# Kernel tuning notes

Hardware: AMD Instinct MI355X
Metric: run time of the kernel (lower is better)

Reference implementation:

```python
import jax, jax.numpy as jnp
import numpy as np

B, L, D, H, HID = 2048, 512, 17, 8, 256  # batch, max entities, feat dim, heads, mlp hidden
SPECIAL, OUT = 9, 23  # special vector dims, policy logits (7+16)


def _lin(k, out_d, in_d, scale):
    kw, kb = jax.random.split(k)
    W = jax.random.normal(kw, (out_d, in_d), jnp.float32) * scale
    b = jax.random.normal(kb, (out_d,), jnp.float32) * 0.01
    return W, b


def setup_inputs() -> dict:
    key = jax.random.key(0)
    ks = jax.random.split(key, 16)
    # observations: row 0 holds the 9-dim special vector, rows 1..L are ragged entities
    x = jax.random.normal(ks[0], (B, L + 1, D), jnp.float32)
    lengths = jax.random.randint(ks[1], (B,), 1, L + 1)
    mask = (jnp.arange(L)[None, :] < lengths[:, None]).astype(jnp.float32)
    x = x.at[:, 1:, :].multiply(mask[:, :, None])  # zero rows mark padding
    s = 1.0 / np.sqrt(D)
    # per-head K/V projections (num_heads separate tiny Linears)
    Wk = jax.random.normal(ks[2], (H, D, D), jnp.float32) * s
    bk = jax.random.normal(ks[3], (H, D), jnp.float32) * 0.01
    Wv = jax.random.normal(ks[4], (H, D, D), jnp.float32) * s
    bv = jax.random.normal(ks[5], (H, D), jnp.float32) * 0.01
    q = jax.random.normal(ks[6], (H, D), jnp.float32)  # learned per-head queries
    Wo, bo = _lin(ks[7], D, H * D, 1.0 / np.sqrt(H * D))
    sc = 1.0 / np.sqrt(D + SPECIAL)
    pW1, pb1 = _lin(ks[8], HID, D + SPECIAL, sc)
    pW2, pb2 = _lin(ks[9], HID, HID, 1.0 / np.sqrt(HID))
    pW3, pb3 = _lin(ks[10], OUT, HID, 1.0 / np.sqrt(HID))
    vW1, vb1 = _lin(ks[11], HID, D + SPECIAL, sc)
    vW2, vb2 = _lin(ks[12], HID, HID, 1.0 / np.sqrt(HID))
    vW3, vb3 = _lin(ks[13], 1, HID, 1.0 / np.sqrt(HID))
    return dict(x=x, Wk=Wk, bk=bk, Wv=Wv, bv=bv, q=q, Wo=Wo, bo=bo,
                pW1=pW1, pb1=pb1, pW2=pW2, pb2=pb2, pW3=pW3, pb3=pb3,
                vW1=vW1, vb1=vb1, vW2=vW2, vb2=vb2, vW3=vW3, vb3=vb3)


def _mlp(h, W1, b1, W2, b2, W3, b3):
    h = jax.nn.relu(h @ W1.T + b1)
    h = jax.nn.relu(h @ W2.T + b2)
    return h @ W3.T + b3


def reference(x, Wk, bk, Wv, bv, q, Wo, bo,
              pW1, pb1, pW2, pb2, pW3, pb3,
              vW1, vb1, vW2, vb2, vW3, vb3):
    special = x[:, 0, :SPECIAL]            # [B, 9]
    seq = x[:, 1:, :]                      # [B, L, D]
    mask = jnp.sum(jnp.abs(seq), axis=-1) != 0  # [B, L] non-padded rows
    # per-head keys/values for all samples at once (batched over the head loop)
    keys = jnp.einsum('bld,hed->bhle', seq, Wk) + bk[None, :, None, :]   # [B,H,L,D]
    vals = jnp.einsum('bld,hed->bhle', seq, Wv) + bv[None, :, None, :]   # [B,H,L,D]
    scores = jnp.einsum('bhle,he->bhl', keys, q)                          # [B,H,L]
    scores = jnp.where(mask[:, None, :], scores, -1e9)
    w = jax.nn.softmax(scores, axis=-1)                                   # [B,H,L]
    agg = jnp.einsum('bhl,bhle->bhe', w, vals).reshape(x.shape[0], H * D)  # concat heads
    attn = agg @ Wo.T + bo                                                # [B, D]
    comb = jnp.concatenate([attn, special], axis=-1)                      # [B, D+9]
    logits = _mlp(comb, pW1, pb1, pW2, pb2, pW3, pb3)                     # [B, 23]
    value = _mlp(comb, vW1, vb1, vW2, vb2, vW3, vb3)                      # [B, 1]
    return logits, value
```

## Files before the change

### kernel.cpp

```cpp
#include <hip/hip_runtime.h>
#include <hip/hip_bf16.h>

#define B_ 2048
#define D_ 17
#define H_ 8
#define HID_ 256
#define OUT_ 23
#define XROW 8721
#define SEQN 8704

__device__ __forceinline__ float4 ld4u(const float* p) {
  float4 v; __builtin_memcpy(&v, p, 16); return v;
}

__global__ __launch_bounds__(256) void prep_kernel(
    const float* __restrict__ pW2, const float* __restrict__ vW2,
    const float* __restrict__ Wk, const float* __restrict__ bk,
    const float* __restrict__ q,
    float* __restrict__ pW2t, float* __restrict__ vW2t, float* __restrict__ qkc)
{
  const int bid = blockIdx.x;
  const int t = threadIdx.x;
  if (bid == 128) {
    if (t < H_ * D_) {
      const int h = t / D_, dd = t - h * D_;
      float s = 0.f;
      #pragma unroll
      for (int e = 0; e < D_; ++e) s = fmaf(Wk[h*289 + e*D_ + dd], q[h*D_ + e], s);
      qkc[h*18 + dd] = s;
    } else if (t < H_ * D_ + H_) {
      const int h = t - H_ * D_;
      float s = 0.f;
      #pragma unroll
      for (int e = 0; e < D_; ++e) s = fmaf(bk[h*D_ + e], q[h*D_ + e], s);
      qkc[h*18 + 17] = s;
    }
    return;
  }
  __shared__ float tile[32][33];
  const int m = bid >> 6, tid = bid & 63;
  const int ti = (tid >> 3) * 32, tk = (tid & 7) * 32;
  const float* src = m ? vW2 : pW2;
  float* dst = m ? vW2t : pW2t;
  const int tx = t & 31, ty = t >> 5;
  #pragma unroll
  for (int r = 0; r < 4; ++r) tile[ty + 8*r][tx] = src[(ti + ty + 8*r)*HID_ + tk + tx];
  __syncthreads();
  #pragma unroll
  for (int r = 0; r < 4; ++r) dst[(tk + ty + 8*r)*HID_ + ti + tx] = tile[tx][ty + 8*r];
}

__global__ __launch_bounds__(256, 4) void attn_comb_kernel(
    const float* __restrict__ x, const float* __restrict__ qkc,
    const float* __restrict__ Wv, const float* __restrict__ bv,
    const float* __restrict__ Wo, const float* __restrict__ bo,
    float* __restrict__ comb)
{
  __shared__ float smem[9688];
  float* s_seq  = smem;
  float* s_part = smem + 8704;
  float* s_swn  = smem + 9280;
  float* s_agg  = smem + 9416;
  float* s_wp   = smem + 9552;

  const int t = threadIdx.x;
  const int b = blockIdx.x;
  const int w = t >> 6, lane = t & 63;
  const int h = lane & 7, rg = lane >> 3;
  const float* xb = x + (size_t)b * XROW;
  const float* xs = xb + D_;

  const float pv = xs[lane * 136];
  unsigned long long live = __ballot(pv != 0.f) | 1ull;
  const int ptop = 63 - __builtin_clzll(live);
  const int nrows = 8 * (ptop + 1);
  const int ng = nrows >> 2;

  {
    const int rounds = (nrows * D_ + 1023) >> 10;
    float4 tmp[9];
    #pragma unroll
    for (int j = 0; j < 9; ++j) {
      if (j < rounds) {
        int off = (j * 256 + t) * 4;
        if (off > SEQN - 4) off = SEQN - 4;
        tmp[j] = ld4u(xs + off);
      }
    }
    #pragma unroll
    for (int j = 0; j < 9; ++j) {
      if (j < rounds) *(float4*)&s_seq[(j * 256 + t) * 4] = tmp[j];
    }
  }

  float qk[D_];
  #pragma unroll
  for (int d = 0; d < D_; ++d) qk[d] = qkc[h*18 + d];
  const float chr = qkc[h*18 + 17];

  __syncthreads();

  float den = 0.f, acc[D_];
  #pragma unroll
  for (int d = 0; d < D_; ++d) acc[d] = 0.f;

  auto dorow = [&](const float* r, bool ok) {
    float sc = chr;
    #pragma unroll
    for (int d = 0; d < D_; ++d) sc = fmaf(qk[d], r[d], sc);
    const float p = (ok && r[0] != 0.f) ? __expf(sc) : 0.f;
    den += p;
    #pragma unroll
    for (int d = 0; d < D_; ++d) acc[d] = fmaf(p, r[d], acc[d]);
  };

  #pragma unroll 1
  for (int g0 = w * 8; g0 < ng; g0 += 32) {
    const int g = g0 + rg;
    const bool okg = (g < ng);
    const float* gb = &s_seq[(okg ? g : (ng - 1)) * 68];
    {
      float fA[36];
      #pragma unroll
      for (int i = 0; i < 9; ++i) {
        const float4 v = *(const float4*)(gb + 4*i);
        fA[4*i] = v.x; fA[4*i+1] = v.y; fA[4*i+2] = v.z; fA[4*i+3] = v.w;
      }
      dorow(&fA[0], okg);
      dorow(&fA[17], okg);
    }
    {
      float fB[36];
      #pragma unroll
      for (int i = 0; i < 9; ++i) {
        const float4 v = *(const float4*)(gb + 32 + 4*i);
        fB[4*i] = v.x; fB[4*i+1] = v.y; fB[4*i+2] = v.z; fB[4*i+3] = v.w;
      }
      dorow(&fB[2], okg);
      dorow(&fB[19], okg);
    }
  }

  #pragma unroll
  for (int m = 8; m <= 32; m <<= 1) {
    den += __shfl_xor(den, m, 64);
    #pragma unroll
    for (int d = 0; d < D_; ++d) acc[d] += __shfl_xor(acc[d], m, 64);
  }
  if (lane < 8) {
    float* pp = &s_part[(w * 8 + lane) * 18];
    pp[0] = den;
    #pragma unroll
    for (int d = 0; d < D_; ++d) pp[1 + d] = acc[d];
  }
  __syncthreads();

  if (t < 136) {
    const int hh = t / D_, d = t - hh * D_;
    float dn = 0.f, ac = 0.f;
    #pragma unroll
    for (int ww = 0; ww < 4; ++ww) {
      const float* pp = &s_part[(ww * 8 + hh) * 18];
      dn += pp[0]; ac += pp[1 + d];
    }
    s_swn[hh * D_ + d] = ac / dn;
  }
  __syncthreads();
  if (t < 136) {
    const int hh = t / D_, e = t - hh * D_;
    float s = bv[hh*D_ + e];
    #pragma unroll
    for (int d = 0; d < D_; ++d) s = fmaf(Wv[hh*289 + e*D_ + d], s_swn[hh*D_ + d], s);
    s_agg[hh*D_ + e] = s;
  }
  __syncthreads();
  if (t < 136) {
    const int o = t >> 3, pt = t & 7;
    float s = 0.f;
    #pragma unroll
    for (int j = 0; j < D_; ++j) s = fmaf(Wo[o*136 + pt*D_ + j], s_agg[pt*D_ + j], s);
    s_wp[t] = s;
  }
  __syncthreads();
  if (t < D_) {
    float s = bo[t];
    #pragma unroll
    for (int pt = 0; pt < 8; ++pt) s += s_wp[t*8 + pt];
    comb[b*26 + t] = s;
  } else if (t < 26) {
    comb[b*26 + t] = xb[t - D_];
  }
}

__global__ __launch_bounds__(512) void mlp_kernel(
    const float* __restrict__ comb,
    const float* __restrict__ pW1, const float* __restrict__ pb1,
    const float* __restrict__ pW2t, const float* __restrict__ pb2,
    const float* __restrict__ pW3, const float* __restrict__ pb3,
    const float* __restrict__ vW1, const float* __restrict__ vb1,
    const float* __restrict__ vW2t, const float* __restrict__ vb2,
    const float* __restrict__ vW3, const float* __restrict__ vb3,
    float* __restrict__ out)
{
  __shared__ float s_comb[8][26];
  __shared__ __align__(16) float s_h1[2][8][HID_];
  __shared__ __align__(16) float s_h2[2][8][HID_];

  const int t = threadIdx.x;
  const int b0 = blockIdx.x * 8;
  const int p = t >> 8;
  const int i = t & 255;

  if (t < 208) { const int bb = t / 26, k = t - bb*26; s_comb[bb][k] = comb[(size_t)(b0 + bb)*26 + k]; }
  __syncthreads();

  const float* W1  = p ? vW1  : pW1;   const float* B1 = p ? vb1 : pb1;
  const float* W2t = p ? vW2t : pW2t;  const float* B2 = p ? vb2 : pb2;

  {
    float a[8];
    #pragma unroll
    for (int bb = 0; bb < 8; ++bb) a[bb] = 0.f;
    const float* wr = W1 + i*26;
    for (int k = 0; k < 26; ++k) {
      const float wk = wr[k];
      #pragma unroll
      for (int bb = 0; bb < 8; ++bb) a[bb] = fmaf(wk, s_comb[bb][k], a[bb]);
    }
    const float bias = B1[i];
    #pragma unroll
    for (int bb = 0; bb < 8; ++bb) s_h1[p][bb][i] = fmaxf(a[bb] + bias, 0.f);
  }
  __syncthreads();

  {
    float a[8];
    #pragma unroll
    for (int bb = 0; bb < 8; ++bb) a[bb] = 0.f;
    #pragma unroll 2
    for (int k4 = 0; k4 < 64; ++k4) {
      const int k = 4*k4;
      const float w0 = W2t[(k    )*HID_ + i];
      const float w1 = W2t[(k + 1)*HID_ + i];
      const float w2 = W2t[(k + 2)*HID_ + i];
      const float w3 = W2t[(k + 3)*HID_ + i];
      #pragma unroll
      for (int bb = 0; bb < 8; ++bb) {
        const float4 hv = *(const float4*)&s_h1[p][bb][k];
        a[bb] = fmaf(w0, hv.x, fmaf(w1, hv.y, fmaf(w2, hv.z, fmaf(w3, hv.w, a[bb]))));
      }
    }
    const float bias = B2[i];
    #pragma unroll
    for (int bb = 0; bb < 8; ++bb) s_h2[p][bb][i] = fmaxf(a[bb] + bias, 0.f);
  }
  __syncthreads();

  if (t < 184) {
    const int bb = t / OUT_, o = t - bb * OUT_;
    const float4* w4 = (const float4*)(pW3 + o * HID_);
    const float4* h4 = (const float4*)&s_h2[0][bb][0];
    float s = pb3[o];
    for (int k = 0; k < 64; ++k) {
      const float4 wv = w4[k], hv = h4[k];
      s = fmaf(wv.x, hv.x, fmaf(wv.y, hv.y, fmaf(wv.z, hv.z, fmaf(wv.w, hv.w, s))));
    }
    out[(size_t)(b0 + bb) * OUT_ + o] = s;
  } else if (t >= 256 && t < 264) {
    const int bb = t - 256;
    const float4* w4 = (const float4*)vW3;
    const float4* h4 = (const float4*)&s_h2[1][bb][0];
    float s = vb3[0];
    for (int k = 0; k < 64; ++k) {
      const float4 wv = w4[k], hv = h4[k];
      s = fmaf(wv.x, hv.x, fmaf(wv.y, hv.y, fmaf(wv.z, hv.z, fmaf(wv.w, hv.w, s))));
    }
    out[(size_t)B_ * OUT_ + b0 + bb] = s;
  }
}

extern "C" void kernel_launch(void* const* d_in, const int* in_sizes, int n_in,
                              void* d_out, int out_size, void* d_ws, size_t ws_size,
                              hipStream_t stream) {
  (void)in_sizes; (void)n_in; (void)out_size; (void)ws_size;
  const float* x   = (const float*)d_in[0];
  const float* Wk  = (const float*)d_in[1];
  const float* bk  = (const float*)d_in[2];
  const float* Wv  = (const float*)d_in[3];
  const float* bv  = (const float*)d_in[4];
  const float* q   = (const float*)d_in[5];
  const float* Wo  = (const float*)d_in[6];
  const float* bo  = (const float*)d_in[7];
  const float* pW1 = (const float*)d_in[8];
  const float* pb1 = (const float*)d_in[9];
  const float* pW2 = (const float*)d_in[10];
  const float* pb2 = (const float*)d_in[11];
  const float* pW3 = (const float*)d_in[12];
  const float* pb3 = (const float*)d_in[13];
  const float* vW1 = (const float*)d_in[14];
  const float* vb1 = (const float*)d_in[15];
  const float* vW2 = (const float*)d_in[16];
  const float* vb2 = (const float*)d_in[17];
  const float* vW3 = (const float*)d_in[18];
  const float* vb3 = (const float*)d_in[19];
  float* out = (float*)d_out;

  float* comb = (float*)d_ws;
  float* pW2t = comb + (size_t)B_ * 26;
  float* vW2t = pW2t + (size_t)HID_ * HID_;
  float* qkc  = vW2t + (size_t)HID_ * HID_;

  prep_kernel<<<129, 256, 0, stream>>>(pW2, vW2, Wk, bk, q, pW2t, vW2t, qkc);
  attn_comb_kernel<<<B_, 256, 0, stream>>>(x, qkc, Wv, bv, Wo, bo, comb);
  mlp_kernel<<<B_ / 8, 512, 0, stream>>>(comb, pW1, pb1, pW2t, pb2, pW3, pb3,
                                         vW1, vb1, vW2t, vb2, vW3, vb3, out);
}
```

Baseline: 57.48 us.

## Batch four samples per attention block with double-buffered loads; restructure MLP layer 2

The attention kernel now handles four samples per 512-thread block. It prefetches the next sample's sequence into registers while computing the current one and writes it into a second shared buffer, so global loads overlap with compute. The MLP second layer is rewritten as split-K. Each wave broadcasts its 64 hidden values through readlane, loads float4 weight columns, and the partial sums are reduced through shared memory. The trade-off is more shared memory and registers per block and fewer blocks in the attention grid, which may lower occupancy.

```diff
diff --git a/kernel.cpp b/kernel.cpp
--- a/kernel.cpp
+++ b/kernel.cpp
@@ -8,9 +8,13 @@
 #define OUT_ 23
 #define XROW 8721
 #define SEQN 8704
+#define NB 4
 
 __device__ __forceinline__ float4 ld4u(const float* p) {
   float4 v; __builtin_memcpy(&v, p, 16); return v;
+}
+__device__ __forceinline__ float bclane(float v, int l) {
+  return __uint_as_float(__builtin_amdgcn_readlane(__float_as_uint(v), l));
 }
 
 __global__ __launch_bounds__(256) void prep_kernel(
@@ -50,47 +54,29 @@
   for (int r = 0; r < 4; ++r) dst[(tk + ty + 8*r)*HID_ + ti + tx] = tile[tx][ty + 8*r];
 }
 
-__global__ __launch_bounds__(256, 4) void attn_comb_kernel(
+__global__ __launch_bounds__(512, 4) void attn_comb_kernel(
     const float* __restrict__ x, const float* __restrict__ qkc,
     const float* __restrict__ Wv, const float* __restrict__ bv,
     const float* __restrict__ Wo, const float* __restrict__ bo,
     float* __restrict__ comb)
 {
-  __shared__ float smem[9688];
-  float* s_seq  = smem;
-  float* s_part = smem + 8704;
-  float* s_swn  = smem + 9280;
-  float* s_agg  = smem + 9416;
-  float* s_wp   = smem + 9552;
+  __shared__ __align__(16) float s_buf[2][SEQN];
+  __shared__ float s_part[8][H_][18];
+  __shared__ float s_swn[H_ * D_];
+  __shared__ float s_agg[H_ * D_];
+  __shared__ float s_wp[136];
+  __shared__ int s_nr[NB];
 
   const int t = threadIdx.x;
-  const int b = blockIdx.x;
   const int w = t >> 6, lane = t & 63;
   const int h = lane & 7, rg = lane >> 3;
-  const float* xb = x + (size_t)b * XROW;
-  const float* xs = xb + D_;
-
-  const float pv = xs[lane * 136];
-  unsigned long long live = __ballot(pv != 0.f) | 1ull;
-  const int ptop = 63 - __builtin_clzll(live);
-  const int nrows = 8 * (ptop + 1);
-  const int ng = nrows >> 2;
-
-  {
-    const int rounds = (nrows * D_ + 1023) >> 10;
-    float4 tmp[9];
-    #pragma unroll
-    for (int j = 0; j < 9; ++j) {
-      if (j < rounds) {
-        int off = (j * 256 + t) * 4;
-        if (off > SEQN - 4) off = SEQN - 4;
-        tmp[j] = ld4u(xs + off);
-      }
-    }
-    #pragma unroll
-    for (int j = 0; j < 9; ++j) {
-      if (j < rounds) *(float4*)&s_seq[(j * 256 + t) * 4] = tmp[j];
-    }
+  const int b0 = blockIdx.x * NB;
+
+  if (w < NB) {
+    const float* xs = x + (size_t)(b0 + w) * XROW + D_;
+    const float pv = xs[lane * 136];
+    unsigned long long live = __ballot(pv != 0.f) | 1ull;
+    if (lane == 0) s_nr[w] = 8 * (64 - __builtin_clzll(live));
   }
 
   float qk[D_];
@@ -100,99 +86,140 @@
 
   __syncthreads();
 
-  float den = 0.f, acc[D_];
-  #pragma unroll
-  for (int d = 0; d < D_; ++d) acc[d] = 0.f;
-
-  auto dorow = [&](const float* r, bool ok) {
-    float sc = chr;
-    #pragma unroll
-    for (int d = 0; d < D_; ++d) sc = fmaf(qk[d], r[d], sc);
-    const float p = (ok && r[0] != 0.f) ? __expf(sc) : 0.f;
-    den += p;
-    #pragma unroll
-    for (int d = 0; d < D_; ++d) acc[d] = fmaf(p, r[d], acc[d]);
-  };
+  {
+    const int rnd = (s_nr[0] * D_ + 2047) >> 11;
+    const float* xs = x + (size_t)b0 * XROW + D_;
+    float4 st[5];
+    #pragma unroll
+    for (int r = 0; r < 5; ++r) if (r < rnd) {
+      int off = ((r << 9) + t) << 2; if (off > SEQN - 4) off = SEQN - 4;
+      st[r] = ld4u(xs + off);
+    }
+    #pragma unroll
+    for (int r = 0; r < 5; ++r) if (r < rnd) {
+      int off = ((r << 9) + t) << 2; if (off > SEQN - 4) off = SEQN - 4;
+      *(float4*)&s_buf[0][off] = st[r];
+    }
+  }
+  __syncthreads();
 
   #pragma unroll 1
-  for (int g0 = w * 8; g0 < ng; g0 += 32) {
-    const int g = g0 + rg;
-    const bool okg = (g < ng);
-    const float* gb = &s_seq[(okg ? g : (ng - 1)) * 68];
+  for (int j = 0; j < NB; ++j) {
+    float4 st[5]; int rnd1 = 0;
+    if (j + 1 < NB) {
+      rnd1 = (s_nr[j+1] * D_ + 2047) >> 11;
+      const float* xs = x + (size_t)(b0 + j + 1) * XROW + D_;
+      #pragma unroll
+      for (int r = 0; r < 5; ++r) if (r < rnd1) {
+        int off = ((r << 9) + t) << 2; if (off > SEQN - 4) off = SEQN - 4;
+        st[r] = ld4u(xs + off);
+      }
+    }
+
+    const int ng = s_nr[j] >> 2;
+    const float* sb = s_buf[j & 1];
+    float den = 0.f, acc[D_];
+    #pragma unroll
+    for (int d = 0; d < D_; ++d) acc[d] = 0.f;
+
+    auto dorow = [&](const float* r, bool ok) {
+      float sc = chr;
+      #pragma unroll
+      for (int d = 0; d < D_; ++d) sc = fmaf(qk[d], r[d], sc);
+      const float p = (ok && r[0] != 0.f) ? __expf(sc) : 0.f;
+      den += p;
+      #pragma unroll
+      for (int d = 0; d < D_; ++d) acc[d] = fmaf(p, r[d], acc[d]);
+    };
+    auto dogran = [&](int g, bool ok) {
+      const float* gb = sb + (ok ? g : 0) * 68;
+      {
+        float f[36];
+        #pragma unroll
+        for (int i = 0; i < 9; ++i) {
+          const float4 v = *(const float4*)(gb + 4*i);
+          f[4*i] = v.x; f[4*i+1] = v.y; f[4*i+2] = v.z; f[4*i+3] = v.w;
+        }
+        dorow(&f[0], ok); dorow(&f[17], ok);
+      }
+      {
+        float f[36];
+        #pragma unroll
+        for (int i = 0; i < 9; ++i) {
+          const float4 v = *(const float4*)(gb + 32 + 4*i);
+          f[4*i] = v.x; f[4*i+1] = v.y; f[4*i+2] = v.z; f[4*i+3] = v.w;
+        }
+        dorow(&f[2], ok); dorow(&f[19], ok);
+      }
+    };
     {
-      float fA[36];
-      #pragma unroll
-      for (int i = 0; i < 9; ++i) {
-        const float4 v = *(const float4*)(gb + 4*i);
-        fA[4*i] = v.x; fA[4*i+1] = v.y; fA[4*i+2] = v.z; fA[4*i+3] = v.w;
-      }
-      dorow(&fA[0], okg);
-      dorow(&fA[17], okg);
-    }
-    {
-      float fB[36];
-      #pragma unroll
-      for (int i = 0; i < 9; ++i) {
-        const float4 v = *(const float4*)(gb + 32 + 4*i);
-        fB[4*i] = v.x; fB[4*i+1] = v.y; fB[4*i+2] = v.z; fB[4*i+3] = v.w;
-      }
-      dorow(&fB[2], okg);
-      dorow(&fB[19], okg);
-    }
-  }
-
-  #pragma unroll
-  for (int m = 8; m <= 32; m <<= 1) {
-    den += __shfl_xor(den, m, 64);
-    #pragma unroll
-    for (int d = 0; d < D_; ++d) acc[d] += __shfl_xor(acc[d], m, 64);
-  }
-  if (lane < 8) {
-    float* pp = &s_part[(w * 8 + lane) * 18];
-    pp[0] = den;
-    #pragma unroll
-    for (int d = 0; d < D_; ++d) pp[1 + d] = acc[d];
-  }
-  __syncthreads();
-
-  if (t < 136) {
-    const int hh = t / D_, d = t - hh * D_;
-    float dn = 0.f, ac = 0.f;
-    #pragma unroll
-    for (int ww = 0; ww < 4; ++ww) {
-      const float* pp = &s_part[(ww * 8 + hh) * 18];
-      dn += pp[0]; ac += pp[1 + d];
-    }
-    s_swn[hh * D_ + d] = ac / dn;
-  }
-  __syncthreads();
-  if (t < 136) {
-    const int hh = t / D_, e = t - hh * D_;
-    float s = bv[hh*D_ + e];
-    #pragma unroll
-    for (int d = 0; d < D_; ++d) s = fmaf(Wv[hh*289 + e*D_ + d], s_swn[hh*D_ + d], s);
-    s_agg[hh*D_ + e] = s;
-  }
-  __syncthreads();
-  if (t < 136) {
-    const int o = t >> 3, pt = t & 7;
-    float s = 0.f;
-    #pragma unroll
-    for (int j = 0; j < D_; ++j) s = fmaf(Wo[o*136 + pt*D_ + j], s_agg[pt*D_ + j], s);
-    s_wp[t] = s;
-  }
-  __syncthreads();
-  if (t < D_) {
-    float s = bo[t];
-    #pragma unroll
-    for (int pt = 0; pt < 8; ++pt) s += s_wp[t*8 + pt];
-    comb[b*26 + t] = s;
-  } else if (t < 26) {
-    comb[b*26 + t] = xb[t - D_];
-  }
-}
-
-__global__ __launch_bounds__(512) void mlp_kernel(
+      const int g = w * 8 + rg;
+      dogran(g, g < ng);
+    }
+    if (w * 8 + 64 < ng) {
+      const int g = w * 8 + rg + 64;
+      dogran(g, g < ng);
+    }
+
+    #pragma unroll
+    for (int m = 8; m <= 32; m <<= 1) {
+      den += __shfl_xor(den, m, 64);
+      #pragma unroll
+      for (int d = 0; d < D_; ++d) acc[d] += __shfl_xor(acc[d], m, 64);
+    }
+    if (lane < 8) {
+      float* pp = &s_part[w][lane][0];
+      pp[0] = den;
+      #pragma unroll
+      for (int d = 0; d < D_; ++d) pp[1 + d] = acc[d];
+    }
+    __syncthreads();
+
+    if (j + 1 < NB) {
+      #pragma unroll
+      for (int r = 0; r < 5; ++r) if (r < rnd1) {
+        int off = ((r << 9) + t) << 2; if (off > SEQN - 4) off = SEQN - 4;
+        *(float4*)&s_buf[(j + 1) & 1][off] = st[r];
+      }
+    }
+
+    if (t < 136) {
+      const int hh = t / D_, d = t - hh * D_;
+      float dn = 0.f, ac = 0.f;
+      #pragma unroll
+      for (int ww = 0; ww < 8; ++ww) { dn += s_part[ww][hh][0]; ac += s_part[ww][hh][1 + d]; }
+      s_swn[hh * D_ + d] = ac / dn;
+    }
+    __syncthreads();
+    if (t < 136) {
+      const int hh = t / D_, e = t - hh * D_;
+      float s = bv[hh*D_ + e];
+      #pragma unroll
+      for (int d = 0; d < D_; ++d) s = fmaf(Wv[hh*289 + e*D_ + d], s_swn[hh*D_ + d], s);
+      s_agg[hh*D_ + e] = s;
+    }
+    __syncthreads();
+    if (t < 136) {
+      const int o = t >> 3, pt = t & 7;
+      float s = 0.f;
+      #pragma unroll
+      for (int jj = 0; jj < D_; ++jj) s = fmaf(Wo[o*136 + pt*D_ + jj], s_agg[pt*D_ + jj], s);
+      s_wp[t] = s;
+    }
+    __syncthreads();
+    if (t < D_) {
+      float s = bo[t];
+      #pragma unroll
+      for (int pt = 0; pt < 8; ++pt) s += s_wp[t*8 + pt];
+      comb[(b0 + j)*26 + t] = s;
+    } else if (t < 26) {
+      comb[(b0 + j)*26 + t] = x[(size_t)(b0 + j) * XROW + (t - D_)];
+    }
+    __syncthreads();
+  }
+}
+
+__global__ __launch_bounds__(512, 2) void mlp_kernel(
     const float* __restrict__ comb,
     const float* __restrict__ pW1, const float* __restrict__ pb1,
     const float* __restrict__ pW2t, const float* __restrict__ pb2,
@@ -203,13 +230,14 @@
     float* __restrict__ out)
 {
   __shared__ float s_comb[8][26];
-  __shared__ __align__(16) float s_h1[2][8][HID_];
+  __shared__ __align__(16) float s_red[2][3][8][HID_];
   __shared__ __align__(16) float s_h2[2][8][HID_];
 
   const int t = threadIdx.x;
   const int b0 = blockIdx.x * 8;
   const int p = t >> 8;
-  const int i = t & 255;
+  const int kq = (t >> 6) & 3;
+  const int ln = t & 63;
 
   if (t < 208) { const int bb = t / 26, k = t - bb*26; s_comb[bb][k] = comb[(size_t)(b0 + bb)*26 + k]; }
   __syncthreads();
@@ -217,11 +245,13 @@
   const float* W1  = p ? vW1  : pW1;   const float* B1 = p ? vb1 : pb1;
   const float* W2t = p ? vW2t : pW2t;  const float* B2 = p ? vb2 : pb2;
 
+  float h[8];
   {
+    const int i = kq * 64 + ln;
     float a[8];
     #pragma unroll
     for (int bb = 0; bb < 8; ++bb) a[bb] = 0.f;
-    const float* wr = W1 + i*26;
+    const float* wr = W1 + i * 26;
     for (int k = 0; k < 26; ++k) {
       const float wk = wr[k];
       #pragma unroll
@@ -229,30 +259,46 @@
     }
     const float bias = B1[i];
     #pragma unroll
-    for (int bb = 0; bb < 8; ++bb) s_h1[p][bb][i] = fmaxf(a[bb] + bias, 0.f);
-  }
-  __syncthreads();
-
+    for (int bb = 0; bb < 8; ++bb) h[bb] = fmaxf(a[bb] + bias, 0.f);
+  }
+
+  float4 acc[8];
+  #pragma unroll
+  for (int bb = 0; bb < 8; ++bb) acc[bb] = make_float4(0.f, 0.f, 0.f, 0.f);
   {
-    float a[8];
-    #pragma unroll
-    for (int bb = 0; bb < 8; ++bb) a[bb] = 0.f;
-    #pragma unroll 2
-    for (int k4 = 0; k4 < 64; ++k4) {
-      const int k = 4*k4;
-      const float w0 = W2t[(k    )*HID_ + i];
-      const float w1 = W2t[(k + 1)*HID_ + i];
-      const float w2 = W2t[(k + 2)*HID_ + i];
-      const float w3 = W2t[(k + 3)*HID_ + i];
+    const float* wbase = W2t + (size_t)(kq * 64) * HID_ + 4 * ln;
+    #pragma unroll 8
+    for (int jj = 0; jj < 64; ++jj) {
+      const float4 wv = *(const float4*)(wbase + (size_t)jj * HID_);
       #pragma unroll
       for (int bb = 0; bb < 8; ++bb) {
-        const float4 hv = *(const float4*)&s_h1[p][bb][k];
-        a[bb] = fmaf(w0, hv.x, fmaf(w1, hv.y, fmaf(w2, hv.z, fmaf(w3, hv.w, a[bb]))));
-      }
-    }
-    const float bias = B2[i];
-    #pragma unroll
-    for (int bb = 0; bb < 8; ++bb) s_h2[p][bb][i] = fmaxf(a[bb] + bias, 0.f);
+        const float hv = bclane(h[bb], jj);
+        acc[bb].x = fmaf(wv.x, hv, acc[bb].x);
+        acc[bb].y = fmaf(wv.y, hv, acc[bb].y);
+        acc[bb].z = fmaf(wv.z, hv, acc[bb].z);
+        acc[bb].w = fmaf(wv.w, hv, acc[bb].w);
+      }
+    }
+  }
+  if (kq > 0) {
+    #pragma unroll
+    for (int bb = 0; bb < 8; ++bb) *(float4*)&s_red[p][kq - 1][bb][4 * ln] = acc[bb];
+  }
+  __syncthreads();
+  if (kq == 0) {
+    const float4 bias = *(const float4*)&B2[4 * ln];
+    #pragma unroll
+    for (int bb = 0; bb < 8; ++bb) {
+      const float4 r0 = *(const float4*)&s_red[p][0][bb][4 * ln];
+      const float4 r1 = *(const float4*)&s_red[p][1][bb][4 * ln];
+      const float4 r2 = *(const float4*)&s_red[p][2][bb][4 * ln];
+      float4 r;
+      r.x = fmaxf(acc[bb].x + r0.x + r1.x + r2.x + bias.x, 0.f);
+      r.y = fmaxf(acc[bb].y + r0.y + r1.y + r2.y + bias.y, 0.f);
+      r.z = fmaxf(acc[bb].z + r0.z + r1.z + r2.z + bias.z, 0.f);
+      r.w = fmaxf(acc[bb].w + r0.w + r1.w + r2.w + bias.w, 0.f);
+      *(float4*)&s_h2[p][bb][4 * ln] = r;
+    }
   }
   __syncthreads();
 
@@ -311,7 +357,7 @@
   float* qkc  = vW2t + (size_t)HID_ * HID_;
 
   prep_kernel<<<129, 256, 0, stream>>>(pW2, vW2, Wk, bk, q, pW2t, vW2t, qkc);
-  attn_comb_kernel<<<B_, 256, 0, stream>>>(x, qkc, Wv, bv, Wo, bo, comb);
+  attn_comb_kernel<<<B_ / NB, 512, 0, stream>>>(x, qkc, Wv, bv, Wo, bo, comb);
   mlp_kernel<<<B_ / 8, 512, 0, stream>>>(comb, pW1, pb1, pW2t, pb2, pW3, pb3,
                                          vW1, vb1, vW2t, vb2, vW3, vb3, out);
 }
```

Result: slower. 70.47 us (+22.6%).
